# Optimization experiments

Measured on AMD Instinct MI355X. Metric: run time of the kernel, lower is better.

## Reference

```python
import jax, jax.numpy as jnp
import numpy as np

B, S, E, H, F = 4, 2048, 1024, 16, 4096
D = E // H
EPS = 1e-5


def setup_inputs() -> dict:
    key = jax.random.key(0)
    ks = jax.random.split(key, 12)
    sc_e = 1.0 / np.sqrt(E)
    sc_f = 1.0 / np.sqrt(F)
    inp = {
        'x': jax.random.normal(ks[0], (B, S, E), jnp.float32),
        'mask': jnp.tril(jnp.ones((S, S), jnp.int32))[None, None],  # causal [1,1,S,S]
        'ln1_g': jnp.ones((E,), jnp.float32),
        'ln1_b': jnp.zeros((E,), jnp.float32),
        'Wq': jax.random.normal(ks[1], (E, E), jnp.float32) * sc_e,
        'bq': jnp.zeros((E,), jnp.float32),
        'Wk': jax.random.normal(ks[2], (E, E), jnp.float32) * sc_e,
        'bk': jnp.zeros((E,), jnp.float32),
        'Wv': jax.random.normal(ks[3], (E, E), jnp.float32) * sc_e,
        'bv': jnp.zeros((E,), jnp.float32),
        'Wo': jax.random.normal(ks[4], (E, E), jnp.float32) * sc_e,
        'bo': jnp.zeros((E,), jnp.float32),
        'ln2_g': jnp.ones((E,), jnp.float32),
        'ln2_b': jnp.zeros((E,), jnp.float32),
        'W1': jax.random.normal(ks[5], (F, E), jnp.float32) * sc_e,
        'b1': jnp.zeros((F,), jnp.float32),
        'W2': jax.random.normal(ks[6], (E, F), jnp.float32) * sc_f,
        'b2': jnp.zeros((E,), jnp.float32),
    }
    return inp


def _ln(x, g, b):
    m = jnp.mean(x, axis=-1, keepdims=True)
    v = jnp.mean(jnp.square(x - m), axis=-1, keepdims=True)
    return (x - m) * jax.lax.rsqrt(v + EPS) * g + b


def _attn(h, mask, Wq, bq, Wk, bk, Wv, bv, Wo, bo):
    b, s, _ = h.shape
    q = (h @ Wq.T + bq).reshape(b, s, H, D)
    k = (h @ Wk.T + bk).reshape(b, s, H, D)
    v = (h @ Wv.T + bv).reshape(b, s, H, D)
    scores = jnp.einsum('bqhd,bkhd->bhqk', q, k) / np.sqrt(D)
    scores = jnp.where(mask == 0, -jnp.inf, scores)
    w = jax.nn.softmax(scores, axis=-1)
    ctx = jnp.einsum('bhqk,bkhd->bqhd', w, v).reshape(b, s, E)
    return ctx @ Wo.T + bo


def reference(x, mask, ln1_g, ln1_b, Wq, bq, Wk, bk, Wv, bv, Wo, bo,
              ln2_g, ln2_b, W1, b1, W2, b2):
    x = x + _attn(_ln(x, ln1_g, ln1_b), mask, Wq, bq, Wk, bk, Wv, bv, Wo, bo)
    h = _ln(x, ln2_g, ln2_b)
    ffn = jax.nn.gelu(h @ W1.T + b1, approximate=False) @ W2.T + b2
    return x + ffn
```

## Files before the change

### kernel.cpp

```cpp
#include <hip/hip_runtime.h>
#include <cstdint>
#include <cstddef>

#define E_DIM 1024
#define F_DIM 4096
#define S_LEN 2048
#define NB    4
#define NH    16
#define HD    64
#define MROWS 8192

typedef __bf16 bf16x8 __attribute__((ext_vector_type(8)));
typedef float  f32x4  __attribute__((ext_vector_type(4)));

struct alignas(16) f4 { float x, y, z, w; };
__device__ __forceinline__ f4 ld4(const float* p){ return *(const f4*)p; }

__device__ __forceinline__ unsigned short f2bf(float f){
  union { float f; unsigned int u; } c; c.f = f;
  unsigned int u = c.u;
  return (unsigned short)((u + 0x7FFFu + ((u >> 16) & 1u)) >> 16);
}

__device__ __forceinline__ float gelu_fast(float v){
  const float x  = v * 0.70710678118654752f;
  const float ax = fabsf(x);
  const float t  = __builtin_amdgcn_rcpf(1.0f + 0.3275911f * ax);
  const float p  = t*(0.254829592f + t*(-0.284496736f + t*(1.421413741f +
                   t*(-1.453152027f + t*1.061405429f))));
  float er = 1.0f - p * __expf(-x * x);
  er = (x < 0.0f) ? -er : er;
  return 0.5f * v * (1.0f + er);
}

__device__ __forceinline__ void xcd_swz(int gx, int gy, int& bn, int& bm){
  int fid = blockIdx.y * gx + blockIdx.x;
  const int nwg = gx * gy;
  fid = (fid & 7) * (nwg >> 3) + (fid >> 3);
  bn = fid % gx; bm = fid / gx;
}

__global__ void cvt_kernel(const float* __restrict__ in, unsigned short* __restrict__ out,
                           int n, float scale){
  int i = (blockIdx.x * 256 + threadIdx.x) * 4;
  if (i >= n) return;
  f4 f = ld4(in + i);
  ushort4 o;
  o.x = f2bf(f.x * scale); o.y = f2bf(f.y * scale);
  o.z = f2bf(f.z * scale); o.w = f2bf(f.w * scale);
  *(ushort4*)(out + i) = o;
}

__global__ void bias_cat(const float* __restrict__ bq, const float* __restrict__ bk,
                         const float* __restrict__ bv, float* __restrict__ out, float qsc){
  int i = blockIdx.x * 256 + threadIdx.x;
  if (i >= 3 * E_DIM) return;
  float v = (i < E_DIM) ? bq[i] * qsc : (i < 2 * E_DIM ? bk[i - E_DIM] : bv[i - 2 * E_DIM]);
  out[i] = v;
}

__global__ __launch_bounds__(256) void ln_kernel(const float* __restrict__ in,
                                                 const float* __restrict__ g,
                                                 const float* __restrict__ b,
                                                 unsigned short* __restrict__ out){
  const int row = blockIdx.x;
  const int t = threadIdx.x;
  const float* xr = in + (size_t)row * E_DIM;
  f4 xv = ld4(xr + t * 4);
  float s  = xv.x + xv.y + xv.z + xv.w;
  float ss = xv.x*xv.x + xv.y*xv.y + xv.z*xv.z + xv.w*xv.w;
  #pragma unroll
  for (int o = 1; o < 64; o <<= 1){ s += __shfl_xor(s, o); ss += __shfl_xor(ss, o); }
  __shared__ float sa[4], sb[4];
  if ((t & 63) == 0){ sa[t >> 6] = s; sb[t >> 6] = ss; }
  __syncthreads();
  s  = sa[0] + sa[1] + sa[2] + sa[3];
  ss = sb[0] + sb[1] + sb[2] + sb[3];
  const float mean = s * (1.0f / E_DIM);
  const float var  = ss * (1.0f / E_DIM) - mean * mean;
  const float rstd = rsqrtf(var + 1e-5f);
  f4 gv = ld4(g + t * 4);
  f4 bv = ld4(b + t * 4);
  ushort4 o;
  o.x = f2bf((xv.x - mean) * rstd * gv.x + bv.x);
  o.y = f2bf((xv.y - mean) * rstd * gv.y + bv.y);
  o.z = f2bf((xv.z - mean) * rstd * gv.z + bv.z);
  o.w = f2bf((xv.w - mean) * rstd * gv.w + bv.w);
  *(ushort4*)(out + (size_t)row * E_DIM + t * 4) = o;
}

__device__ __forceinline__ void async_cp16(const unsigned short* g, unsigned short* l){
  __builtin_amdgcn_global_load_lds((const __attribute__((address_space(1))) unsigned int*)g,
                                   (__attribute__((address_space(3)))       unsigned int*)l,
                                   16, 0, 0);
}

#define VMW4() asm volatile("s_waitcnt vmcnt(4)" ::: "memory")
#define VMW0() asm volatile("s_waitcnt vmcnt(0)" ::: "memory")
#define BAR()  __builtin_amdgcn_s_barrier()

template<int EPI>
__global__ __launch_bounds__(512, 2) void gemm256(const unsigned short* __restrict__ A,
                                                  const unsigned short* __restrict__ W,
                                                  const float* __restrict__ bias,
                                                  unsigned short* __restrict__ outp,
                                                  int M, int N, int K){
  __shared__ unsigned short lds[2][2][256 * 64];
  const int bn = blockIdx.x, bm = blockIdx.y;
  const int tid = threadIdx.x;
  const int lane = tid & 63;
  const int wv = tid >> 6;
  const int lr = lane & 15, qd = lane >> 4;
  const int wm = wv >> 2, wn = wv & 3;
  const int NT = K >> 6;

  f32x4 acc[2][2][4][2];
  #pragma unroll
  for (int a = 0; a < 2; ++a)
    #pragma unroll
    for (int b = 0; b < 2; ++b)
      #pragma unroll
      for (int c = 0; c < 4; ++c)
        #pragma unroll
        for (int d = 0; d < 2; ++d)
          acc[a][b][c][d] = f32x4{0.f, 0.f, 0.f, 0.f};

  const int srow = tid >> 3;
  const int scol = ((tid & 7) ^ (srow & 7)) * 8;
  const unsigned short* Ab = A + (size_t)(bm * 256 + srow) * K + scol;
  const unsigned short* Wb = W + (size_t)(bn * 256 + srow) * K + scol;

#define STAGE_A(bufi, h, kt) do{ \
    async_cp16(Ab + (size_t)((h)*128     ) * K + (size_t)(kt) * 64, &lds[bufi][0][((h)*128     ) * 64 + tid * 8]); \
    async_cp16(Ab + (size_t)((h)*128 + 64) * K + (size_t)(kt) * 64, &lds[bufi][0][((h)*128 + 64) * 64 + tid * 8]); \
  }while(0)
#define STAGE_B(bufi, h, kt) do{ \
    async_cp16(Wb + (size_t)((h)*128     ) * K + (size_t)(kt) * 64, &lds[bufi][1][((h)*128     ) * 64 + tid * 8]); \
    async_cp16(Wb + (size_t)((h)*128 + 64) * K + (size_t)(kt) * 64, &lds[bufi][1][((h)*128 + 64) * 64 + tid * 8]); \
  }while(0)

  const int sw0 = ((qd    ) ^ (lr & 7)) * 8;
  const int sw1 = ((qd + 4) ^ (lr & 7)) * 8;
  const int arow = wm * 64 + lr;
  const int brow = wn * 32 + lr;

  bf16x8 af[4][2], b0[2][2], b1[2][2];

#define LDA(bufi, mh) do{ \
    _Pragma("unroll") \
    for (int mt = 0; mt < 4; ++mt){ \
      const int r_ = (mh)*128 + arow + mt * 16; \
      af[mt][0] = *(const bf16x8*)&lds[bufi][0][r_ * 64 + sw0]; \
      af[mt][1] = *(const bf16x8*)&lds[bufi][0][r_ * 64 + sw1]; \
    } }while(0)
#define LDB(bufi, nh, dst) do{ \
    _Pragma("unroll") \
    for (int nt = 0; nt < 2; ++nt){ \
      const int r_ = (nh)*128 + brow + nt * 16; \
      dst[nt][0] = *(const bf16x8*)&lds[bufi][1][r_ * 64 + sw0]; \
      dst[nt][1] = *(const bf16x8*)&lds[bufi][1][r_ * 64 + sw1]; \
    } }while(0)
#define MMA(mh, nh, bfr) do{ \
    __builtin_amdgcn_s_setprio(1); \
    _Pragma("unroll") \
    for (int kk = 0; kk < 2; ++kk) \
      _Pragma("unroll") \
      for (int mt = 0; mt < 4; ++mt) \
        _Pragma("unroll") \
        for (int nt = 0; nt < 2; ++nt) \
          acc[mh][nh][mt][nt] = __builtin_amdgcn_mfma_f32_16x16x32_bf16(af[mt][kk], bfr[nt][kk], acc[mh][nh][mt][nt], 0, 0, 0); \
    __builtin_amdgcn_s_setprio(0); \
  }while(0)

  STAGE_A(0, 0, 0); STAGE_B(0, 1, 0); STAGE_A(0, 1, 0); STAGE_B(0, 0, 0);
  STAGE_A(1, 0, 1); STAGE_B(1, 1, 1);
  VMW4(); BAR();

  for (int t = 0; t < NT; t += 2){
    const bool s2 = (t + 2) < NT, s3 = (t + 3) < NT;
    LDA(0, 0); LDB(0, 0, b0);
    STAGE_A(1, 1, t + 1);
    BAR(); MMA(0, 0, b0);
    LDB(0, 1, b1);
    BAR();
    STAGE_B(1, 0, t + 1);
    BAR(); MMA(0, 1, b1);
    LDA(0, 1);
    BAR();
    if (s2) STAGE_A(0, 0, t + 2);
    BAR(); MMA(1, 1, b1); BAR();
    if (s2) STAGE_B(0, 1, t + 2);
    BAR(); MMA(1, 0, b0);
    if (s2) { VMW4(); } else { VMW0(); }
    LDA(1, 0);
    BAR();
    LDB(1, 0, b0);
    if (s2) STAGE_A(0, 1, t + 2);
    BAR(); MMA(0, 0, b0);
    LDB(1, 1, b1);
    BAR();
    if (s2) STAGE_B(0, 0, t + 2);
    BAR(); MMA(0, 1, b1);
    LDA(1, 1);
    BAR();
    if (s3) STAGE_A(1, 0, t + 3);
    BAR(); MMA(1, 1, b1); BAR();
    if (s3) STAGE_B(1, 1, t + 3);
    BAR(); MMA(1, 0, b0);
    VMW4();
    BAR();
  }

  #pragma unroll
  for (int mh = 0; mh < 2; ++mh)
    #pragma unroll
    for (int nh = 0; nh < 2; ++nh)
      #pragma unroll
      for (int mt = 0; mt < 4; ++mt){
        const int gm0 = bm * 256 + mh * 128 + wm * 64 + mt * 16 + qd * 4;
        #pragma unroll
        for (int r = 0; r < 4; ++r){
          const size_t rowoff = (size_t)(gm0 + r) * N;
          #pragma unroll
          for (int nt = 0; nt < 2; ++nt){
            const int gn = bn * 256 + nh * 128 + wn * 32 + nt * 16 + lr;
            float v = acc[mh][nh][mt][nt][r] + bias[gn];
            if constexpr (EPI == 1) v = gelu_fast(v);
            outp[rowoff + gn] = f2bf(v);
          }
        }
      }
#undef STAGE_A
#undef STAGE_B
#undef LDA
#undef LDB
#undef MMA
}

__global__ __launch_bounds__(512, 1) void gemm256x128(const unsigned short* __restrict__ A,
                                                      const unsigned short* __restrict__ W,
                                                      const float* __restrict__ bias,
                                                      const float* __restrict__ res,
                                                      float* __restrict__ outp,
                                                      int M, int N, int K){
  __shared__ unsigned short As[2][256 * 64];
  __shared__ unsigned short Bs[2][128 * 64];
  int bn, bm; xcd_swz(gridDim.x, gridDim.y, bn, bm);
  const int tid = threadIdx.x;
  const int lane = tid & 63;
  const int wv = tid >> 6;
  const int lr = lane & 15, qd = lane >> 4;
  const int wm = wv >> 1, wn = wv & 1;
  const int NT = K >> 6;

  f32x4 acc[4][4];
  #pragma unroll
  for (int a = 0; a < 4; ++a)
    #pragma unroll
    for (int b = 0; b < 4; ++b)
      acc[a][b] = f32x4{0.f, 0.f, 0.f, 0.f};

  const int srow = tid >> 3;
  const int scol = ((tid & 7) ^ (srow & 7)) * 8;
  const int sdst = srow * 64 + (tid & 7) * 8;
  const unsigned short* Ab = A + (size_t)(bm * 256 + srow) * K + scol;
  const unsigned short* Wb = W + (size_t)(bn * 128 + srow) * K + scol;

#define XSTAGE_A(bufi, kt) do{ \
    _Pragma("unroll") \
    for (int h = 0; h < 4; ++h) \
      async_cp16(Ab + (size_t)(h * 64) * K + (size_t)(kt) * 64, &As[bufi][h * 64 * 64 + sdst]); \
  }while(0)
#define XSTAGE_B(bufi, kt) do{ \
    _Pragma("unroll") \
    for (int h = 0; h < 2; ++h) \
      async_cp16(Wb + (size_t)(h * 64) * K + (size_t)(kt) * 64, &Bs[bufi][h * 64 * 64 + sdst]); \
  }while(0)

  const int sw0 = ((qd    ) ^ (lr & 7)) * 8;
  const int sw1 = ((qd + 4) ^ (lr & 7)) * 8;
  const int arow = wm * 64 + lr;
  const int brow = wn * 64 + lr;

  bf16x8 af[4][2], b0[2][2], b1[2][2];

#define XLDA(bufi) do{ \
    _Pragma("unroll") \
    for (int mt = 0; mt < 4; ++mt){ \
      const int r_ = arow + mt * 16; \
      af[mt][0] = *(const bf16x8*)&As[bufi][r_ * 64 + sw0]; \
      af[mt][1] = *(const bf16x8*)&As[bufi][r_ * 64 + sw1]; \
    } }while(0)
#define XLDB0(bufi) do{ \
    _Pragma("unroll") \
    for (int j = 0; j < 2; ++j){ \
      const int r_ = brow + j * 16; \
      b0[j][0] = *(const bf16x8*)&Bs[bufi][r_ * 64 + sw0]; \
      b0[j][1] = *(const bf16x8*)&Bs[bufi][r_ * 64 + sw1]; \
    } }while(0)
#define XLDB1(bufi) do{ \
    _Pragma("unroll") \
    for (int j = 0; j < 2; ++j){ \
      const int r_ = brow + (2 + j) * 16; \
      b1[j][0] = *(const bf16x8*)&Bs[bufi][r_ * 64 + sw0]; \
      b1[j][1] = *(const bf16x8*)&Bs[bufi][r_ * 64 + sw1]; \
    } }while(0)
#define XMMA0() do{ \
    __builtin_amdgcn_s_setprio(1); \
    _Pragma("unroll") \
    for (int kk = 0; kk < 2; ++kk) \
      _Pragma("unroll") \
      for (int mt = 0; mt < 4; ++mt) \
        _Pragma("unroll") \
        for (int j = 0; j < 2; ++j) \
          acc[mt][j] = __builtin_amdgcn_mfma_f32_16x16x32_bf16(af[mt][kk], b0[j][kk], acc[mt][j], 0, 0, 0); \
    __builtin_amdgcn_s_setprio(0); \
  }while(0)
#define XMMA1() do{ \
    __builtin_amdgcn_s_setprio(1); \
    _Pragma("unroll") \
    for (int kk = 0; kk < 2; ++kk) \
      _Pragma("unroll") \
      for (int mt = 0; mt < 4; ++mt) \
        _Pragma("unroll") \
        for (int j = 0; j < 2; ++j) \
          acc[mt][2 + j] = __builtin_amdgcn_mfma_f32_16x16x32_bf16(af[mt][kk], b1[j][kk], acc[mt][2 + j], 0, 0, 0); \
    __builtin_amdgcn_s_setprio(0); \
  }while(0)

  XSTAGE_A(0, 0); XSTAGE_B(0, 0); XSTAGE_A(1, 1);
  VMW4(); BAR();

  for (int t = 0; t < NT; t += 2){
    const bool s2 = (t + 2) < NT;
    XLDA(0); XLDB0(0);
    XSTAGE_B(1, t + 1);
    BAR(); XMMA0();
    XLDB1(0);
    BAR();
    if (s2) XSTAGE_A(0, t + 2);
    BAR(); XMMA1();
    if (s2) { VMW4(); } else { VMW0(); }
    XLDA(1); XLDB0(1);
    BAR();
    if (s2) XSTAGE_B(0, t + 2);
    BAR(); XMMA0();
    XLDB1(1);
    BAR();
    if (s2) XSTAGE_A(1, t + 3);
    BAR(); XMMA1();
    if (s2) VMW4();
    BAR();
  }

  #pragma unroll
  for (int mt = 0; mt < 4; ++mt){
    #pragma unroll
    for (int r = 0; r < 4; ++r){
      const int gm = bm * 256 + wm * 64 + mt * 16 + qd * 4 + r;
      const size_t rowoff = (size_t)gm * N;
      #pragma unroll
      for (int nt = 0; nt < 4; ++nt){
        const int gn = bn * 128 + wn * 64 + nt * 16 + lr;
        const float v = acc[mt][nt][r] + bias[gn];
        outp[rowoff + gn] = v + res[rowoff + gn];
      }
    }
  }
#undef XSTAGE_A
#undef XSTAGE_B
#undef XLDA
#undef XLDB0
#undef XLDB1
#undef XMMA0
#undef XMMA1
}

__global__ __launch_bounds__(256) void vtrans(const unsigned short* __restrict__ QKV,
                                              unsigned short* __restrict__ Vt){
  __shared__ unsigned short Ts[64 * 66];
  const int st = blockIdx.x;
  const int h = blockIdx.y, b = blockIdx.z;
  const int tid = threadIdx.x;
  const size_t srcbase = (size_t)(b * S_LEN + st * 64) * 3072 + 2 * E_DIM + h * HD;
  #pragma unroll
  for (int it = 0; it < 4; ++it){
    const int ch = tid + it * 256;
    const int row = ch >> 4, c4 = (ch & 15) * 4;
    *(ushort4*)&Ts[row * 66 + c4] = *(const ushort4*)(QKV + srcbase + (size_t)row * 3072 + c4);
  }
  __syncthreads();
  const size_t dstbase = (size_t)((b * NH + h) * HD) * S_LEN + st * 64;
  #pragma unroll
  for (int it = 0; it < 4; ++it){
    const int ch = tid + it * 256;
    const int d = ch >> 4, t4 = (ch & 15) * 4;
    ushort4 o;
    o.x = Ts[(t4 + 0) * 66 + d];
    o.y = Ts[(t4 + 1) * 66 + d];
    o.z = Ts[(t4 + 2) * 66 + d];
    o.w = Ts[(t4 + 3) * 66 + d];
    *(ushort4*)&Vt[dstbase + (size_t)d * S_LEN + t4] = o;
  }
}

#define AST 72
__global__ __launch_bounds__(256) void attn_mfma(const unsigned short* __restrict__ QKV,
                                                 const unsigned short* __restrict__ Vt,
                                                 unsigned short* __restrict__ Om){
  __shared__ unsigned short Ks[64 * 64];
  __shared__ unsigned short Vs[64 * 64];
  __shared__ unsigned short Ps[64 * AST];
  const int pairi = blockIdx.x;
  const int h = blockIdx.y, b = blockIdx.z;
  const int tid = threadIdx.x;
  const int w = tid >> 6, lane = tid & 63;
  const int lr = lane & 15, qd = lane >> 4;
  const size_t row0 = (size_t)b * S_LEN;
  const int qcol = h * HD;
  const int kcol = E_DIM + h * HD;
  const unsigned short* Vtb = Vt + (size_t)((b * NH + h) * HD) * S_LEN;

  const int sr  = tid >> 3;
  const int sc  = (((tid & 7) ^ (sr & 7))) * 8;
  const int sdst = sr * 64 + (tid & 7) * 8;

  bf16x8 ones;
  #pragma unroll
  for (int j = 0; j < 8; ++j) ones[j] = (__bf16)1.0f;

  for (int ph = 0; ph < 2; ++ph){
    const int qb_t = ph ? (31 - pairi) : pairi;
    const int q0 = qb_t * 64 + w * 16;

    bf16x8 qf[2];
    #pragma unroll
    for (int kk = 0; kk < 2; ++kk)
      qf[kk] = *(const bf16x8*)(QKV + (row0 + q0 + lr) * 3072 + qcol + kk * 32 + qd * 8);

    f32x4 accd[4];
    #pragma unroll
    for (int dt = 0; dt < 4; ++dt) accd[dt] = f32x4{0.f, 0.f, 0.f, 0.f};
    f32x4 lacc = f32x4{0.f, 0.f, 0.f, 0.f};

    uint4 k0r = *(const uint4*)(QKV + (row0 + sr) * 3072 + kcol + sc);
    uint4 k1r = *(const uint4*)(QKV + (row0 + sr + 32) * 3072 + kcol + sc);
    uint4 v0r = *(const uint4*)(Vtb + (size_t)sr * S_LEN + sc);
    uint4 v1r = *(const uint4*)(Vtb + (size_t)(sr + 32) * S_LEN + sc);

    for (int kt = 0; kt <= qb_t; ++kt){
      __syncthreads();
      *(uint4*)&Ks[sdst          ] = k0r;
      *(uint4*)&Ks[sdst + 32 * 64] = k1r;
      *(uint4*)&Vs[sdst          ] = v0r;
      *(uint4*)&Vs[sdst + 32 * 64] = v1r;
      if (kt < qb_t){
        const int kn = kt + 1;
        k0r = *(const uint4*)(QKV + (row0 + kn * 64 + sr) * 3072 + kcol + sc);
        k1r = *(const uint4*)(QKV + (row0 + kn * 64 + sr + 32) * 3072 + kcol + sc);
        v0r = *(const uint4*)(Vtb + (size_t)sr * S_LEN + kn * 64 + sc);
        v1r = *(const uint4*)(Vtb + (size_t)(sr + 32) * S_LEN + kn * 64 + sc);
      }
      __syncthreads();

      f32x4 s[4];
      #pragma unroll
      for (int nt = 0; nt < 4; ++nt) s[nt] = f32x4{0.f, 0.f, 0.f, 0.f};
      #pragma unroll
      for (int kk = 0; kk < 2; ++kk){
        bf16x8 kf[4];
        #pragma unroll
        for (int nt = 0; nt < 4; ++nt)
          kf[nt] = *(const bf16x8*)&Ks[(nt * 16 + lr) * 64 + (((kk * 4 + qd) ^ (lr & 7))) * 8];
        #pragma unroll
        for (int nt = 0; nt < 4; ++nt)
          s[nt] = __builtin_amdgcn_mfma_f32_16x16x32_bf16(qf[kk], kf[nt], s[nt], 0, 0, 0);
      }
      if (kt == qb_t){
        #pragma unroll
        for (int nt = 0; nt < 4; ++nt)
          #pragma unroll
          for (int r = 0; r < 4; ++r){
            const int q  = q0 + qd * 4 + r;
            const int ky = kt * 64 + nt * 16 + lr;
            if (ky > q) s[nt][r] = -3e38f;
          }
      }
      #pragma unroll
      for (int nt = 0; nt < 4; ++nt)
        #pragma unroll
        for (int r = 0; r < 4; ++r){
          union { float f; unsigned u; } cc;
          cc.f = exp2f(s[nt][r]);
          Ps[(w * 16 + qd * 4 + r) * AST + nt * 16 + lr] = (unsigned short)((cc.u + 0x8000u) >> 16);
        }
      __builtin_amdgcn_s_waitcnt(0xc07f);
      #pragma unroll
      for (int kk = 0; kk < 2; ++kk){
        bf16x8 pf = *(const bf16x8*)&Ps[(w * 16 + lr) * AST + kk * 32 + qd * 8];
        bf16x8 vf[4];
        #pragma unroll
        for (int dt = 0; dt < 4; ++dt)
          vf[dt] = *(const bf16x8*)&Vs[(dt * 16 + lr) * 64 + (((kk * 4 + qd) ^ (lr & 7))) * 8];
        #pragma unroll
        for (int dt = 0; dt < 4; ++dt)
          accd[dt] = __builtin_amdgcn_mfma_f32_16x16x32_bf16(pf, vf[dt], accd[dt], 0, 0, 0);
        lacc = __builtin_amdgcn_mfma_f32_16x16x32_bf16(pf, ones, lacc, 0, 0, 0);
      }
    }

    #pragma unroll
    for (int r = 0; r < 4; ++r){
      const float inv = 1.0f / lacc[r];
      const size_t ro = (row0 + q0 + qd * 4 + r) * E_DIM + qcol;
      #pragma unroll
      for (int dt = 0; dt < 4; ++dt)
        Om[ro + dt * 16 + lr] = f2bf(accd[dt][r] * inv);
    }
  }
}

extern "C" void kernel_launch(void* const* d_in, const int* in_sizes, int n_in,
                              void* d_out, int out_size, void* d_ws, size_t ws_size,
                              hipStream_t stream){
  const float* x    = (const float*)d_in[0];
  const float* ln1g = (const float*)d_in[2];
  const float* ln1b = (const float*)d_in[3];
  const float* Wq   = (const float*)d_in[4];
  const float* bq   = (const float*)d_in[5];
  const float* Wk   = (const float*)d_in[6];
  const float* bk   = (const float*)d_in[7];
  const float* Wv   = (const float*)d_in[8];
  const float* bv   = (const float*)d_in[9];
  const float* Wo   = (const float*)d_in[10];
  const float* bo   = (const float*)d_in[11];
  const float* ln2g = (const float*)d_in[12];
  const float* ln2b = (const float*)d_in[13];
  const float* W1   = (const float*)d_in[14];
  const float* b1   = (const float*)d_in[15];
  const float* W2   = (const float*)d_in[16];
  const float* b2   = (const float*)d_in[17];

  char* ws = (char*)d_ws;
  const size_t MB = 1024 * 1024;
  unsigned short* Wqkv_b = (unsigned short*)(ws + 0 * MB);
  unsigned short* Wo_b   = (unsigned short*)(ws + 6 * MB);
  unsigned short* W1_b   = (unsigned short*)(ws + 8 * MB);
  unsigned short* W2_b   = (unsigned short*)(ws + 16 * MB);
  unsigned short* qkvb   = (unsigned short*)(ws + 24 * MB);
  float*          bqkv   = (float*)(ws + 72 * MB);
  unsigned short* Vt_g   = (unsigned short*)(ws + 72 * MB);
  unsigned short* lnb    = (unsigned short*)(ws + 88 * MB);
  float*          xres   = (float*)(ws + 104 * MB);
  unsigned short* ffn1   = (unsigned short*)(ws + 24 * MB);
  unsigned short* ctxb   = lnb;

  const float QSC = 0.125f * 1.4426950408889634f;

  cvt_kernel<<<1024, 256, 0, stream>>>(Wq, Wqkv_b,                   E_DIM * E_DIM, QSC);
  cvt_kernel<<<1024, 256, 0, stream>>>(Wk, Wqkv_b + E_DIM * E_DIM,   E_DIM * E_DIM, 1.0f);
  cvt_kernel<<<1024, 256, 0, stream>>>(Wv, Wqkv_b + 2 * E_DIM * E_DIM, E_DIM * E_DIM, 1.0f);
  cvt_kernel<<<1024, 256, 0, stream>>>(Wo, Wo_b, E_DIM * E_DIM, 1.0f);
  cvt_kernel<<<4096, 256, 0, stream>>>(W1, W1_b, F_DIM * E_DIM, 1.0f);
  cvt_kernel<<<4096, 256, 0, stream>>>(W2, W2_b, F_DIM * E_DIM, 1.0f);
  bias_cat<<<12, 256, 0, stream>>>(bq, bk, bv, bqkv, QSC);

  ln_kernel<<<MROWS, 256, 0, stream>>>(x, ln1g, ln1b, lnb);

  gemm256<0><<<dim3(3 * E_DIM / 256, MROWS / 256), 512, 0, stream>>>(
      lnb, Wqkv_b, bqkv, qkvb, MROWS, 3 * E_DIM, E_DIM);

  vtrans<<<dim3(S_LEN / 64, NH, NB), 256, 0, stream>>>(qkvb, Vt_g);

  attn_mfma<<<dim3(16, NH, NB), 256, 0, stream>>>(qkvb, Vt_g, ctxb);

  gemm256x128<<<dim3(E_DIM / 128, MROWS / 256), 512, 0, stream>>>(
      ctxb, Wo_b, bo, x, xres, MROWS, E_DIM, E_DIM);

  ln_kernel<<<MROWS, 256, 0, stream>>>(xres, ln2g, ln2b, lnb);

  gemm256<1><<<dim3(F_DIM / 256, MROWS / 256), 512, 0, stream>>>(
      lnb, W1_b, b1, ffn1, MROWS, F_DIM, E_DIM);

  gemm256x128<<<dim3(E_DIM / 128, MROWS / 256), 512, 0, stream>>>(
      ffn1, W2_b, b2, xres, (float*)d_out, MROWS, E_DIM, F_DIM);
}
```

Before: 528.5 us.

## Enlarge attention query tile to 128 rows and merge weight conversion kernels

Each attention block now processes 128 query rows, with each wave handling two 16-row sub-tiles. Every K/V tile staged in shared memory is therefore reused for twice as many queries, and the grid is halved. Causal masking is applied per sub-tile wherever a key tile overlaps the diagonal. The six weight conversion kernels and the bias concatenation are merged into one launch to cut launch overhead. The changes raise register and LDS use and reduce block-level parallelism, which may hurt occupancy and load balance.

```diff
diff --git a/kernel.cpp b/kernel.cpp
--- a/kernel.cpp
+++ b/kernel.cpp
@@ -40,23 +40,36 @@
   bn = fid % gx; bm = fid / gx;
 }
 
-__global__ void cvt_kernel(const float* __restrict__ in, unsigned short* __restrict__ out,
-                           int n, float scale){
-  int i = (blockIdx.x * 256 + threadIdx.x) * 4;
-  if (i >= n) return;
-  f4 f = ld4(in + i);
-  ushort4 o;
-  o.x = f2bf(f.x * scale); o.y = f2bf(f.y * scale);
-  o.z = f2bf(f.z * scale); o.w = f2bf(f.w * scale);
-  *(ushort4*)(out + i) = o;
-}
-
-__global__ void bias_cat(const float* __restrict__ bq, const float* __restrict__ bk,
-                         const float* __restrict__ bv, float* __restrict__ out, float qsc){
-  int i = blockIdx.x * 256 + threadIdx.x;
-  if (i >= 3 * E_DIM) return;
-  float v = (i < E_DIM) ? bq[i] * qsc : (i < 2 * E_DIM ? bk[i - E_DIM] : bv[i - 2 * E_DIM]);
-  out[i] = v;
+__global__ void cvt_all(const float* __restrict__ Wq, const float* __restrict__ Wk,
+                        const float* __restrict__ Wv, const float* __restrict__ Wo,
+                        const float* __restrict__ W1, const float* __restrict__ W2,
+                        const float* __restrict__ bq, const float* __restrict__ bk,
+                        const float* __restrict__ bv,
+                        unsigned short* __restrict__ Wqkv_b, unsigned short* __restrict__ Wo_b,
+                        unsigned short* __restrict__ W1_b, unsigned short* __restrict__ W2_b,
+                        float* __restrict__ bqkv, float qsc){
+  const int blk = blockIdx.x;
+  if (blk < 12288){
+    const float* src; unsigned short* dst; float scale = 1.0f; int base;
+    if      (blk < 1024){ src = Wq; dst = Wqkv_b;                 base = blk;        scale = qsc; }
+    else if (blk < 2048){ src = Wk; dst = Wqkv_b + 1024 * 1024;   base = blk - 1024; }
+    else if (blk < 3072){ src = Wv; dst = Wqkv_b + 2048 * 1024;   base = blk - 2048; }
+    else if (blk < 4096){ src = Wo; dst = Wo_b;                   base = blk - 3072; }
+    else if (blk < 8192){ src = W1; dst = W1_b;                   base = blk - 4096; }
+    else                { src = W2; dst = W2_b;                   base = blk - 8192; }
+    const int i = (base * 256 + threadIdx.x) * 4;
+    f4 f = ld4(src + i);
+    ushort4 o;
+    o.x = f2bf(f.x * scale); o.y = f2bf(f.y * scale);
+    o.z = f2bf(f.z * scale); o.w = f2bf(f.w * scale);
+    *(ushort4*)(dst + i) = o;
+  } else {
+    const int i = (blk - 12288) * 256 + threadIdx.x;
+    if (i < 3 * E_DIM){
+      float v = (i < E_DIM) ? bq[i] * qsc : (i < 2 * E_DIM ? bk[i - E_DIM] : bv[i - 2 * E_DIM]);
+      bqkv[i] = v;
+    }
+  }
 }
 
 __global__ __launch_bounds__(256) void ln_kernel(const float* __restrict__ in,
@@ -410,7 +423,7 @@
                                                  unsigned short* __restrict__ Om){
   __shared__ unsigned short Ks[64 * 64];
   __shared__ unsigned short Vs[64 * 64];
-  __shared__ unsigned short Ps[64 * AST];
+  __shared__ unsigned short Ps[128 * AST];
   const int pairi = blockIdx.x;
   const int h = blockIdx.y, b = blockIdx.z;
   const int tid = threadIdx.x;
@@ -430,31 +443,38 @@
   for (int j = 0; j < 8; ++j) ones[j] = (__bf16)1.0f;
 
   for (int ph = 0; ph < 2; ++ph){
-    const int qb_t = ph ? (31 - pairi) : pairi;
-    const int q0 = qb_t * 64 + w * 16;
-
-    bf16x8 qf[2];
+    const int qt = ph ? (15 - pairi) : pairi;
+    const int q0 = qt * 128 + w * 32;
+    const int nkt = 2 * qt + 2;
+
+    bf16x8 qf[2][2];
     #pragma unroll
-    for (int kk = 0; kk < 2; ++kk)
-      qf[kk] = *(const bf16x8*)(QKV + (row0 + q0 + lr) * 3072 + qcol + kk * 32 + qd * 8);
-
-    f32x4 accd[4];
+    for (int qs = 0; qs < 2; ++qs)
+      #pragma unroll
+      for (int kk = 0; kk < 2; ++kk)
+        qf[qs][kk] = *(const bf16x8*)(QKV + (row0 + q0 + qs * 16 + lr) * 3072 + qcol + kk * 32 + qd * 8);
+
+    f32x4 accd[2][4];
     #pragma unroll
-    for (int dt = 0; dt < 4; ++dt) accd[dt] = f32x4{0.f, 0.f, 0.f, 0.f};
-    f32x4 lacc = f32x4{0.f, 0.f, 0.f, 0.f};
+    for (int qs = 0; qs < 2; ++qs)
+      #pragma unroll
+      for (int dt = 0; dt < 4; ++dt) accd[qs][dt] = f32x4{0.f, 0.f, 0.f, 0.f};
+    f32x4 lacc[2];
+    lacc[0] = f32x4{0.f, 0.f, 0.f, 0.f};
+    lacc[1] = f32x4{0.f, 0.f, 0.f, 0.f};
 
     uint4 k0r = *(const uint4*)(QKV + (row0 + sr) * 3072 + kcol + sc);
     uint4 k1r = *(const uint4*)(QKV + (row0 + sr + 32) * 3072 + kcol + sc);
     uint4 v0r = *(const uint4*)(Vtb + (size_t)sr * S_LEN + sc);
     uint4 v1r = *(const uint4*)(Vtb + (size_t)(sr + 32) * S_LEN + sc);
 
-    for (int kt = 0; kt <= qb_t; ++kt){
+    for (int kt = 0; kt < nkt; ++kt){
       __syncthreads();
       *(uint4*)&Ks[sdst          ] = k0r;
       *(uint4*)&Ks[sdst + 32 * 64] = k1r;
       *(uint4*)&Vs[sdst          ] = v0r;
       *(uint4*)&Vs[sdst + 32 * 64] = v1r;
-      if (kt < qb_t){
+      if (kt + 1 < nkt){
         const int kn = kt + 1;
         k0r = *(const uint4*)(QKV + (row0 + kn * 64 + sr) * 3072 + kcol + sc);
         k1r = *(const uint4*)(QKV + (row0 + kn * 64 + sr + 32) * 3072 + kcol + sc);
@@ -463,9 +483,11 @@
       }
       __syncthreads();
 
-      f32x4 s[4];
-      #pragma unroll
-      for (int nt = 0; nt < 4; ++nt) s[nt] = f32x4{0.f, 0.f, 0.f, 0.f};
+      f32x4 s[2][4];
+      #pragma unroll
+      for (int qs = 0; qs < 2; ++qs)
+        #pragma unroll
+        for (int nt = 0; nt < 4; ++nt) s[qs][nt] = f32x4{0.f, 0.f, 0.f, 0.f};
       #pragma unroll
       for (int kk = 0; kk < 2; ++kk){
         bf16x8 kf[4];
@@ -473,50 +495,62 @@
         for (int nt = 0; nt < 4; ++nt)
           kf[nt] = *(const bf16x8*)&Ks[(nt * 16 + lr) * 64 + (((kk * 4 + qd) ^ (lr & 7))) * 8];
         #pragma unroll
-        for (int nt = 0; nt < 4; ++nt)
-          s[nt] = __builtin_amdgcn_mfma_f32_16x16x32_bf16(qf[kk], kf[nt], s[nt], 0, 0, 0);
+        for (int qs = 0; qs < 2; ++qs)
+          #pragma unroll
+          for (int nt = 0; nt < 4; ++nt)
+            s[qs][nt] = __builtin_amdgcn_mfma_f32_16x16x32_bf16(qf[qs][kk], kf[nt], s[qs][nt], 0, 0, 0);
       }
-      if (kt == qb_t){
+      #pragma unroll
+      for (int qs = 0; qs < 2; ++qs){
+        if (kt * 64 + 63 > q0 + qs * 16){
+          #pragma unroll
+          for (int nt = 0; nt < 4; ++nt)
+            #pragma unroll
+            for (int r = 0; r < 4; ++r){
+              const int q  = q0 + qs * 16 + qd * 4 + r;
+              const int ky = kt * 64 + nt * 16 + lr;
+              if (ky > q) s[qs][nt][r] = -3e38f;
+            }
+        }
+      }
+      #pragma unroll
+      for (int qs = 0; qs < 2; ++qs)
         #pragma unroll
         for (int nt = 0; nt < 4; ++nt)
           #pragma unroll
           for (int r = 0; r < 4; ++r){
-            const int q  = q0 + qd * 4 + r;
-            const int ky = kt * 64 + nt * 16 + lr;
-            if (ky > q) s[nt][r] = -3e38f;
+            union { float f; unsigned u; } cc;
+            cc.f = exp2f(s[qs][nt][r]);
+            Ps[(w * 32 + qs * 16 + qd * 4 + r) * AST + nt * 16 + lr] = (unsigned short)((cc.u + 0x8000u) >> 16);
           }
-      }
-      #pragma unroll
-      for (int nt = 0; nt < 4; ++nt)
-        #pragma unroll
-        for (int r = 0; r < 4; ++r){
-          union { float f; unsigned u; } cc;
-          cc.f = exp2f(s[nt][r]);
-          Ps[(w * 16 + qd * 4 + r) * AST + nt * 16 + lr] = (unsigned short)((cc.u + 0x8000u) >> 16);
-        }
       __builtin_amdgcn_s_waitcnt(0xc07f);
       #pragma unroll
       for (int kk = 0; kk < 2; ++kk){
-        bf16x8 pf = *(const bf16x8*)&Ps[(w * 16 + lr) * AST + kk * 32 + qd * 8];
         bf16x8 vf[4];
         #pragma unroll
         for (int dt = 0; dt < 4; ++dt)
           vf[dt] = *(const bf16x8*)&Vs[(dt * 16 + lr) * 64 + (((kk * 4 + qd) ^ (lr & 7))) * 8];
         #pragma unroll
-        for (int dt = 0; dt < 4; ++dt)
-          accd[dt] = __builtin_amdgcn_mfma_f32_16x16x32_bf16(pf, vf[dt], accd[dt], 0, 0, 0);
-        lacc = __builtin_amdgcn_mfma_f32_16x16x32_bf16(pf, ones, lacc, 0, 0, 0);
+        for (int qs = 0; qs < 2; ++qs){
+          bf16x8 pf = *(const bf16x8*)&Ps[(w * 32 + qs * 16 + lr) * AST + kk * 32 + qd * 8];
+          #pragma unroll
+          for (int dt = 0; dt < 4; ++dt)
+            accd[qs][dt] = __builtin_amdgcn_mfma_f32_16x16x32_bf16(pf, vf[dt], accd[qs][dt], 0, 0, 0);
+          lacc[qs] = __builtin_amdgcn_mfma_f32_16x16x32_bf16(pf, ones, lacc[qs], 0, 0, 0);
+        }
       }
     }
 
     #pragma unroll
-    for (int r = 0; r < 4; ++r){
-      const float inv = 1.0f / lacc[r];
-      const size_t ro = (row0 + q0 + qd * 4 + r) * E_DIM + qcol;
-      #pragma unroll
-      for (int dt = 0; dt < 4; ++dt)
-        Om[ro + dt * 16 + lr] = f2bf(accd[dt][r] * inv);
-    }
+    for (int qs = 0; qs < 2; ++qs)
+      #pragma unroll
+      for (int r = 0; r < 4; ++r){
+        const float inv = 1.0f / lacc[qs][r];
+        const size_t ro = (row0 + q0 + qs * 16 + qd * 4 + r) * E_DIM + qcol;
+        #pragma unroll
+        for (int dt = 0; dt < 4; ++dt)
+          Om[ro + dt * 16 + lr] = f2bf(accd[qs][dt][r] * inv);
+      }
   }
 }
 
@@ -557,13 +591,8 @@
 
   const float QSC = 0.125f * 1.4426950408889634f;
 
-  cvt_kernel<<<1024, 256, 0, stream>>>(Wq, Wqkv_b,                   E_DIM * E_DIM, QSC);
-  cvt_kernel<<<1024, 256, 0, stream>>>(Wk, Wqkv_b + E_DIM * E_DIM,   E_DIM * E_DIM, 1.0f);
-  cvt_kernel<<<1024, 256, 0, stream>>>(Wv, Wqkv_b + 2 * E_DIM * E_DIM, E_DIM * E_DIM, 1.0f);
-  cvt_kernel<<<1024, 256, 0, stream>>>(Wo, Wo_b, E_DIM * E_DIM, 1.0f);
-  cvt_kernel<<<4096, 256, 0, stream>>>(W1, W1_b, F_DIM * E_DIM, 1.0f);
-  cvt_kernel<<<4096, 256, 0, stream>>>(W2, W2_b, F_DIM * E_DIM, 1.0f);
-  bias_cat<<<12, 256, 0, stream>>>(bq, bk, bv, bqkv, QSC);
+  cvt_all<<<12300, 256, 0, stream>>>(Wq, Wk, Wv, Wo, W1, W2, bq, bk, bv,
+                                     Wqkv_b, Wo_b, W1_b, W2_b, bqkv, QSC);
 
   ln_kernel<<<MROWS, 256, 0, stream>>>(x, ln1g, ln1b, lnb);
 
@@ -572,7 +601,7 @@
 
   vtrans<<<dim3(S_LEN / 64, NH, NB), 256, 0, stream>>>(qkvb, Vt_g);
 
-  attn_mfma<<<dim3(16, NH, NB), 256, 0, stream>>>(qkvb, Vt_g, ctxb);
+  attn_mfma<<<dim3(8, NH, NB), 256, 0, stream>>>(qkvb, Vt_g, ctxb);
 
   gemm256x128<<<dim3(E_DIM / 128, MROWS / 256), 512, 0, stream>>>(
       ctxb, Wo_b, bo, x, xres, MROWS, E_DIM, E_DIM);
```

New measurement: 502.2 us. -5.0%, faster.
